# Performance work log

Measured on AMD Instinct MI355X. Metric: run time of the kernel, lower is better.

The kernel has to match this reference:

```python
import jax, jax.numpy as jnp
import numpy as np

N_POINTS = 16
SPHERE_RADIUS = 2.5
BIG = 1e9

def _layernorm(x, g, b, eps=1e-5):
    mu = jnp.mean(x, axis=-1, keepdims=True)
    var = jnp.var(x, axis=-1, keepdims=True)
    return (x - mu) * jax.lax.rsqrt(var + eps) * g + b

def setup_inputs() -> dict:
    key = jax.random.key(0)
    ks = jax.random.split(key, 12)
    R, I, D, L = 1048576, 8, 64, 2
    orig = jax.random.normal(ks[0], (R, 3), jnp.float32)
    vec = jax.random.normal(ks[1], (R, 3), jnp.float32)
    vec = vec / jnp.linalg.norm(vec, axis=-1, keepdims=True)
    t1 = jax.random.uniform(ks[2], (I, R), jnp.float32) * 2.0
    t2 = t1 + jax.random.uniform(ks[3], (I, R), jnp.float32) * 0.5
    mask = jax.random.randint(ks[4], (I, R), 0, 2) > 0
    W_in = jax.random.normal(ks[5], (N_POINTS * 3, D), jnp.float32) * 0.1
    b_in = jnp.zeros((D,), jnp.float32)
    ln_g = jnp.ones((L, D), jnp.float32)
    ln_b = jnp.zeros((L, D), jnp.float32)
    W_mid = jax.random.normal(ks[6], (L, D, D), jnp.float32) * 0.1
    b_mid = jnp.zeros((L, D), jnp.float32)
    W_cls = jax.random.normal(ks[7], (D, 1), jnp.float32) * 0.1
    b_cls = jnp.zeros((1,), jnp.float32)
    W_dist = jax.random.normal(ks[8], (D, 1), jnp.float32) * 0.1
    b_dist = jnp.zeros((1,), jnp.float32)
    return dict(orig=orig, vec=vec, t1=t1, t2=t2, mask=mask,
                W_in=W_in, b_in=b_in, ln_g=ln_g, ln_b=ln_b,
                W_mid=W_mid, b_mid=b_mid, W_cls=W_cls, b_cls=b_cls,
                W_dist=W_dist, b_dist=b_dist)

def reference(orig, vec, t1, t2, mask, W_in, b_in, ln_g, ln_b, W_mid, b_mid,
              W_cls, b_cls, W_dist, b_dist):
    R = orig.shape[0]
    L = W_mid.shape[0]
    ts = jnp.linspace(0.0, 1.0, N_POINTS)  # [P]

    def net(x):  # x: [R, P*3]
        h = x @ W_in + b_in
        for l in range(L):
            h = jax.nn.relu(h)
            h = _layernorm(h, ln_g[l], ln_b[l])
            h = h @ W_mid[l] + b_mid[l]
        h = jax.nn.relu(h)
        cls = (h @ W_cls + b_cls)[:, 0]
        dval = (h @ W_dist + b_dist)[:, 0]
        return cls, dval

    def step(dist, it):
        m_i, t1_i, t2_i = it  # [R]
        dt = t2_i - t1_i
        inp_orig = orig + vec * t1_i[:, None]          # [R,3]
        inp_vec = vec * dt[:, None]                    # [R,3]
        # sample points along segment: [R, P, 3]
        inp = (inp_orig[:, None, :] + inp_vec[:, None, :] * ts[None, :, None]) / SPHERE_RADIUS
        cls, dval = net(inp.reshape(R, -1))
        dval = dval * dt + t1_i
        upd = (cls > 0) & (dval < dist) & m_i
        return jnp.where(upd, dval, dist), None

    dist0 = jnp.full((R,), BIG, jnp.float32)
    dist, _ = jax.lax.scan(step, dist0, (mask, t1, t2))
    dist = jnp.where(dist == BIG, 0.0, dist)
    return (dist > 0, dist)
```

## Files before the change

kernel.cpp:

```cpp
#include <hip/hip_runtime.h>
#include <math.h>

constexpr int   P      = 16;
constexpr int   DIN    = 48;
constexpr int   DH     = 64;
constexpr int   NITER  = 8;
constexpr int   NLAYER = 2;
constexpr float BIGV   = 1e9f;
constexpr float INV_R  = 1.0f / 2.5f;
constexpr int   RLOG   = 20;

typedef float f32x4 __attribute__((ext_vector_type(4)));
typedef const __attribute__((address_space(1))) f32x4 gf4_t;

__device__ __forceinline__ gf4_t* vmem(const float* p) {
    unsigned long long a = (unsigned long long)p;
    asm volatile("" : "+v"(a));
    return (gf4_t*)a;
}

__device__ __forceinline__ unsigned fkey(float f) {
    unsigned b = __float_as_uint(f);
    return (b & 0x80000000u) ? ~b : (b | 0x80000000u);
}
__device__ __forceinline__ float funkey(unsigned k) {
    unsigned b = (k & 0x80000000u) ? (k ^ 0x80000000u) : ~k;
    return __uint_as_float(b);
}

__device__ __noinline__
void slow_eval(const float* __restrict__ orig, const float* __restrict__ vec,
               const float* __restrict__ t1,   const float* __restrict__ t2,
               size_t tidx, unsigned r,
               const float* __restrict__ W_in,  const float* __restrict__ b_in,
               const float* __restrict__ ln_g,  const float* __restrict__ ln_b,
               const float* __restrict__ W_mid, const float* __restrict__ b_mid,
               const float* __restrict__ W_cls, const float* __restrict__ b_cls,
               const float* __restrict__ W_dist,const float* __restrict__ b_dist,
               float& cls_o, float& dval_o)
{
    const float o0 = orig[3*r+0], o1 = orig[3*r+1], o2 = orig[3*r+2];
    const float v0 = vec[3*r+0],  v1 = vec[3*r+1],  v2 = vec[3*r+2];
    const float t1i = t1[tidx], t2i = t2[tidx];

    const float dt  = __fsub_rn(t2i, t1i);
    const float io0 = __fadd_rn(o0, __fmul_rn(v0, t1i));
    const float io1 = __fadd_rn(o1, __fmul_rn(v1, t1i));
    const float io2 = __fadd_rn(o2, __fmul_rn(v2, t1i));
    const float iv0 = __fmul_rn(v0, dt);
    const float iv1 = __fmul_rn(v1, dt);
    const float iv2 = __fmul_rn(v2, dt);
    const float delta = 1.0f / 15.0f;

    float x[DIN];
    #pragma unroll
    for (int p = 0; p < P; ++p) {
        const float tp = __fmul_rn((float)p, delta);
        x[3*p+0] = __fdiv_rn(__fadd_rn(io0, __fmul_rn(iv0, tp)), 2.5f);
        x[3*p+1] = __fdiv_rn(__fadd_rn(io1, __fmul_rn(iv1, tp)), 2.5f);
        x[3*p+2] = __fdiv_rn(__fadd_rn(io2, __fmul_rn(iv2, tp)), 2.5f);
    }

    float a[DH];
    #pragma unroll 1
    for (int d = 0; d < DH; ++d) {
        double acc0 = 0.0, acc1 = 0.0;
        #pragma unroll
        for (int k = 0; k < DIN; k += 2) {
            acc0 = fma((double)x[k],   (double)W_in[k*DH + d],     acc0);
            acc1 = fma((double)x[k+1], (double)W_in[(k+1)*DH + d], acc1);
        }
        a[d] = __fadd_rn((float)(acc0 + acc1), b_in[d]);
    }

    #pragma unroll 1
    for (int l = 0; l < NLAYER; ++l) {
        #pragma unroll 1
        for (int d = 0; d < DH; ++d) a[d] = fmaxf(a[d], 0.0f);

        double s = 0.0;
        #pragma unroll 1
        for (int d = 0; d < DH; ++d) s += (double)a[d];
        const float mu = (float)(s * (1.0 / 64.0));

        double vs = 0.0;
        #pragma unroll 1
        for (int d = 0; d < DH; ++d) {
            const float c = __fsub_rn(a[d], mu);
            vs = fma((double)c, (double)c, vs);
        }
        const float var = (float)(vs * (1.0 / 64.0));
        const float ve  = __fadd_rn(var, 1e-5f);
        const float inv = (float)(1.0 / sqrt((double)ve));

        float hn[DH];
        #pragma unroll 1
        for (int d = 0; d < DH; ++d) {
            float t = __fsub_rn(a[d], mu);
            t = __fmul_rn(t, inv);
            t = __fmul_rn(t, ln_g[l*DH + d]);
            hn[d] = __fadd_rn(t, ln_b[l*DH + d]);
        }

        #pragma unroll 1
        for (int d = 0; d < DH; ++d) {
            double acc0 = 0.0, acc1 = 0.0;
            #pragma unroll
            for (int k = 0; k < DH; k += 2) {
                acc0 = fma((double)hn[k],   (double)W_mid[(l*DH + k)*DH + d],   acc0);
                acc1 = fma((double)hn[k+1], (double)W_mid[(l*DH + k+1)*DH + d], acc1);
            }
            a[d] = __fadd_rn((float)(acc0 + acc1), b_mid[l*DH + d]);
        }
    }

    double c0 = 0.0, c1 = 0.0, d0 = 0.0, d1 = 0.0;
    #pragma unroll 1
    for (int d = 0; d < DH; d += 2) {
        const float h0 = fmaxf(a[d],   0.0f);
        const float h1 = fmaxf(a[d+1], 0.0f);
        c0 = fma((double)h0, (double)W_cls[d],    c0);
        c1 = fma((double)h1, (double)W_cls[d+1],  c1);
        d0 = fma((double)h0, (double)W_dist[d],   d0);
        d1 = fma((double)h1, (double)W_dist[d+1], d1);
    }
    const float cls = __fadd_rn((float)(c0 + c1), b_cls[0]);
    const float dv  = __fadd_rn((float)(d0 + d1), b_dist[0]);
    cls_o  = cls;
    dval_o = __fadd_rn(__fmul_rn(dv, dt), t1i);
}

__global__ __launch_bounds__(256)
void compact_k(const int* __restrict__ mask, unsigned* __restrict__ cnt,
               unsigned* __restrict__ work)
{
    __shared__ unsigned wcnt[4];
    __shared__ unsigned woff[4];

    const int tid  = threadIdx.x;
    const int lane = tid & 63;
    const int wv   = tid >> 6;
    const int idx  = blockIdx.x * 256 + tid;

    const bool m = (mask[idx] != 0);
    const unsigned long long b = __ballot(m);
    const int nact = __popcll(b);
    if (lane == 0) wcnt[wv] = (unsigned)nact;
    __syncthreads();
    if (tid == 0) {
        const unsigned tot = wcnt[0] + wcnt[1] + wcnt[2] + wcnt[3];
        unsigned base = tot ? atomicAdd(cnt, tot) : 0u;
        #pragma unroll
        for (int w = 0; w < 4; ++w) { woff[w] = base; base += wcnt[w]; }
    }
    __syncthreads();
    if (m) {
        const int pre = __popcll(b & ((1ull << lane) - 1ull));
        work[woff[wv] + pre] = (unsigned)idx;
    }
}

__global__ __launch_bounds__(256)
void init_k(unsigned* __restrict__ arena, int R)
{
    const unsigned key_big = fkey(BIGV);
    for (int r = blockIdx.x * 256 + threadIdx.x; r < R; r += gridDim.x * 256)
        arena[r] = key_big;
}

__global__ __launch_bounds__(256)
void finalize_k(float* __restrict__ out, int R)
{
    unsigned* arena = (unsigned*)out + R;
    for (int r = blockIdx.x * 256 + threadIdx.x; r < R; r += gridDim.x * 256) {
        const float dist = funkey(arena[r]);
        const float dfin = (dist == BIGV) ? 0.0f : dist;
        out[r] = (dfin > 0.0f) ? 1.0f : 0.0f;
        ((float*)arena)[r] = dfin;
    }
}

template<bool GLOBAL>
__device__ __forceinline__
void mm_khalf1(const float* Wbase, int kofs, const float* col, float (&a)[DH])
{
    #pragma unroll 2
    for (int k = 0; k < 32; ++k) {
        const float hk = col[k*64];
        if constexpr (GLOBAL) {
            gf4_t* wr = vmem(Wbase + (kofs + k)*DH);
            #pragma unroll
            for (int j = 0; j < 16; ++j) {
                const f32x4 w4 = wr[j];
                a[4*j+0] = fmaf(hk, w4.x, a[4*j+0]);
                a[4*j+1] = fmaf(hk, w4.y, a[4*j+1]);
                a[4*j+2] = fmaf(hk, w4.z, a[4*j+2]);
                a[4*j+3] = fmaf(hk, w4.w, a[4*j+3]);
            }
        } else {
            const f32x4* wr = (const f32x4*)(Wbase + (kofs + k)*DH);
            #pragma unroll
            for (int j = 0; j < 16; ++j) {
                const f32x4 w4 = wr[j];
                a[4*j+0] = fmaf(hk, w4.x, a[4*j+0]);
                a[4*j+1] = fmaf(hk, w4.y, a[4*j+1]);
                a[4*j+2] = fmaf(hk, w4.z, a[4*j+2]);
                a[4*j+3] = fmaf(hk, w4.w, a[4*j+3]);
            }
        }
    }
}

__global__ __launch_bounds__(256, 3)
void main1_k(const float* __restrict__ orig,
             const float* __restrict__ vec,
             const float* __restrict__ t1,
             const float* __restrict__ t2,
             const float* __restrict__ W_in,
             const float* __restrict__ b_in,
             const float* __restrict__ ln_g,
             const float* __restrict__ ln_b,
             const float* __restrict__ W_mid,
             const float* __restrict__ b_mid,
             const float* __restrict__ W_cls,
             const float* __restrict__ b_cls,
             const float* __restrict__ W_dist,
             const float* __restrict__ b_dist,
             const unsigned* __restrict__ work,
             const unsigned* __restrict__ cnt,
             unsigned* __restrict__ arena)
{
    __shared__ __align__(16) float wl0[DH*DH];
    __shared__ __align__(16) float act[4][32][64];

    const int tid  = threadIdx.x;
    const int lane = tid & 63;
    const int wv   = tid >> 6;

    {
        f32x4*       dst = (f32x4*)wl0;
        const f32x4* s2  = (const f32x4*)W_mid;
        #pragma unroll 1
        for (int idx = tid; idx < DH*DH/4; idx += 256) dst[idx] = s2[idx];
    }
    __syncthreads();

    float* col = &act[wv][0][lane];

    const unsigned T    = *cnt;
    const unsigned gtid = blockIdx.x * 256 + tid;
    const unsigned NTOT = gridDim.x * 256;

    for (unsigned g = gtid; g < T; g += NTOT) {
        const unsigned pk = work[g];
        const unsigned r  = pk & 0xFFFFFu;
        const float tt1 = t1[pk], tt2 = t2[pk];
        const float dt  = tt2 - tt1;
        const float o0 = orig[3*r+0], o1 = orig[3*r+1], o2 = orig[3*r+2];
        const float v0 = vec[3*r+0],  v1 = vec[3*r+1],  v2 = vec[3*r+2];
        const float io0 = fmaf(v0, tt1, o0);
        const float io1 = fmaf(v1, tt1, o1);
        const float io2 = fmaf(v2, tt1, o2);
        const float iv0 = v0 * dt, iv1 = v1 * dt, iv2 = v2 * dt;

        float a[DH];
        #pragma unroll
        for (int d = 0; d < DH; ++d) a[d] = 0.0f;

        #pragma unroll 1
        for (int p = 0; p < P; ++p) {
            const float tp = (float)p * (1.0f / 15.0f);
            const float x0 = fmaf(iv0, tp, io0) * INV_R;
            const float x1 = fmaf(iv1, tp, io1) * INV_R;
            const float x2 = fmaf(iv2, tp, io2) * INV_R;
            gf4_t* w0 = vmem(W_in + (3*p+0)*DH);
            gf4_t* w1 = vmem(W_in + (3*p+1)*DH);
            gf4_t* w2 = vmem(W_in + (3*p+2)*DH);
            #pragma unroll
            for (int j = 0; j < 16; ++j) {
                const f32x4 u = w0[j], v4 = w1[j], w4 = w2[j];
                a[4*j+0] = fmaf(x2, w4.x, fmaf(x1, v4.x, fmaf(x0, u.x, a[4*j+0])));
                a[4*j+1] = fmaf(x2, w4.y, fmaf(x1, v4.y, fmaf(x0, u.y, a[4*j+1])));
                a[4*j+2] = fmaf(x2, w4.z, fmaf(x1, v4.z, fmaf(x0, u.z, a[4*j+2])));
                a[4*j+3] = fmaf(x2, w4.w, fmaf(x1, v4.w, fmaf(x0, u.w, a[4*j+3])));
            }
        }
        #pragma unroll
        for (int d = 0; d < DH; ++d) a[d] += b_in[d];

        float invprod = 1.0f;

        #pragma unroll
        for (int l = 0; l < NLAYER; ++l) {
            #pragma unroll
            for (int d = 0; d < DH; ++d) a[d] = fmaxf(a[d], 0.0f);

            float mu = 0.0f;
            #pragma unroll
            for (int d = 0; d < DH; ++d) mu += a[d];
            mu *= (1.0f / 64.0f);

            float var = 0.0f;
            #pragma unroll
            for (int d = 0; d < DH; ++d) {
                const float c = a[d] - mu;
                var = fmaf(c, c, var);
            }
            var *= (1.0f / 64.0f);
            const float inv = 1.0f / sqrtf(var + 1e-5f);
            invprod *= inv;

            const float* gg = ln_g + l*DH;
            const float* bb = ln_b + l*DH;

            #pragma unroll
            for (int d = 0; d < 32; ++d)
                col[d*64] = fmaf((a[d] - mu) * inv, gg[d], bb[d]);
            float hh[32];
            #pragma unroll
            for (int j = 0; j < 32; ++j)
                hh[j] = fmaf((a[32+j] - mu) * inv, gg[32+j], bb[32+j]);

            #pragma unroll
            for (int d = 0; d < DH; ++d) a[d] = 0.0f;

            if (l == 0) mm_khalf1<false>(wl0,            0, col, a);
            else        mm_khalf1<true >(W_mid + DH*DH,  0, col, a);

            #pragma unroll
            for (int j = 0; j < 32; ++j)
                col[j*64] = hh[j];

            if (l == 0) mm_khalf1<false>(wl0,           32, col, a);
            else        mm_khalf1<true >(W_mid + DH*DH, 32, col, a);

            const float* bm = b_mid + l*DH;
            #pragma unroll
            for (int d = 0; d < DH; ++d) a[d] += bm[d];
        }

        #pragma unroll
        for (int d = 0; d < DH; ++d) a[d] = fmaxf(a[d], 0.0f);

        float c0 = 0.f, c1 = 0.f, c2 = 0.f, c3 = 0.f;
        float e0 = 0.f, e1 = 0.f, e2 = 0.f, e3 = 0.f;
        #pragma unroll
        for (int j = 0; j < 16; ++j) {
            c0 = fmaf(a[4*j+0], W_cls[4*j+0],  c0);
            c1 = fmaf(a[4*j+1], W_cls[4*j+1],  c1);
            c2 = fmaf(a[4*j+2], W_cls[4*j+2],  c2);
            c3 = fmaf(a[4*j+3], W_cls[4*j+3],  c3);
            e0 = fmaf(a[4*j+0], W_dist[4*j+0], e0);
            e1 = fmaf(a[4*j+1], W_dist[4*j+1], e1);
            e2 = fmaf(a[4*j+2], W_dist[4*j+2], e2);
            e3 = fmaf(a[4*j+3], W_dist[4*j+3], e3);
        }
        float cls = ((c0 + c1) + (c2 + c3)) + b_cls[0];
        float dv  = ((e0 + e1) + (e2 + e3)) + b_dist[0];
        float dval = fmaf(dv, dt, tt1);

        float thr = 2e-6f * invprod;
        thr = fminf(fmaxf(thr, 3e-5f), 2e-2f);
        if ((fabsf(cls) < thr) || (fabsf(dval) < thr)) {
            slow_eval(orig, vec, t1, t2, (size_t)pk, r,
                      W_in, b_in, ln_g, ln_b, W_mid, b_mid,
                      W_cls, b_cls, W_dist, b_dist, cls, dval);
        }
        if (cls > 0.0f)
            atomicMin(arena + r, fkey(dval));
    }
}

__global__ __launch_bounds__(256, 2)
void fallback_k(const float* __restrict__ orig, const float* __restrict__ vec,
                const float* __restrict__ t1,   const float* __restrict__ t2,
                const int*   __restrict__ mask,
                const float* __restrict__ W_in,  const float* __restrict__ b_in,
                const float* __restrict__ ln_g,  const float* __restrict__ ln_b,
                const float* __restrict__ W_mid, const float* __restrict__ b_mid,
                const float* __restrict__ W_cls, const float* __restrict__ b_cls,
                const float* __restrict__ W_dist,const float* __restrict__ b_dist,
                float* __restrict__ out, int R)
{
    __shared__ __align__(16) float wlds[DIN*DH + NLAYER*DH*DH];
    __shared__ __align__(16) float act[4][32][64];

    const int tid  = threadIdx.x;
    const int lane = tid & 63;
    const int wv   = tid >> 6;

    {
        f32x4*       dst = (f32x4*)wlds;
        const f32x4* s1  = (const f32x4*)W_in;
        const f32x4* s2  = (const f32x4*)W_mid;
        #pragma unroll 1
        for (int idx = tid; idx < DIN*DH/4; idx += 256)        dst[idx] = s1[idx];
        #pragma unroll 1
        for (int idx = tid; idx < NLAYER*DH*DH/4; idx += 256)  dst[DIN*DH/4 + idx] = s2[idx];
    }
    __syncthreads();

    const float* win_l  = wlds;
    const float* wmid_l = wlds + DIN*DH;

    const int r = blockIdx.x * 256 + tid;
    if (r >= R) return;

    float* myact = &act[wv][0][lane];

    const float o0 = orig[3*r+0], o1 = orig[3*r+1], o2 = orig[3*r+2];
    const float v0 = vec[3*r+0],  v1 = vec[3*r+1],  v2 = vec[3*r+2];

    float dist = BIGV;

    #pragma unroll 1
    for (int i = 0; i < NITER; ++i) {
        const float t1i = t1[(size_t)i * R + r];
        const float t2i = t2[(size_t)i * R + r];
        const int   mi  = mask[(size_t)i * R + r];
        if (!mi) continue;
        const float dt = t2i - t1i;

        const float io0 = fmaf(v0, t1i, o0);
        const float io1 = fmaf(v1, t1i, o1);
        const float io2 = fmaf(v2, t1i, o2);
        const float iv0 = v0 * dt, iv1 = v1 * dt, iv2 = v2 * dt;

        float a[DH];
        #pragma unroll
        for (int d = 0; d < DH; ++d) a[d] = 0.0f;

        #pragma unroll 1
        for (int p = 0; p < P; ++p) {
            const float tp = (float)p * (1.0f / 15.0f);
            const float x0 = fmaf(iv0, tp, io0) * INV_R;
            const float x1 = fmaf(iv1, tp, io1) * INV_R;
            const float x2 = fmaf(iv2, tp, io2) * INV_R;
            const f32x4* w0 = (const f32x4*)(win_l + (3*p+0)*DH);
            const f32x4* w1 = (const f32x4*)(win_l + (3*p+1)*DH);
            const f32x4* w2 = (const f32x4*)(win_l + (3*p+2)*DH);
            #pragma unroll
            for (int j = 0; j < 16; ++j) {
                const f32x4 u = w0[j], v4 = w1[j], w4 = w2[j];
                a[4*j+0] = fmaf(x2, w4.x, fmaf(x1, v4.x, fmaf(x0, u.x, a[4*j+0])));
                a[4*j+1] = fmaf(x2, w4.y, fmaf(x1, v4.y, fmaf(x0, u.y, a[4*j+1])));
                a[4*j+2] = fmaf(x2, w4.z, fmaf(x1, v4.z, fmaf(x0, u.z, a[4*j+2])));
                a[4*j+3] = fmaf(x2, w4.w, fmaf(x1, v4.w, fmaf(x0, u.w, a[4*j+3])));
            }
        }
        #pragma unroll
        for (int d = 0; d < DH; ++d) a[d] += b_in[d];

        float invprod = 1.0f;

        #pragma unroll 1
        for (int l = 0; l < NLAYER; ++l) {
            #pragma unroll
            for (int d = 0; d < DH; ++d) a[d] = fmaxf(a[d], 0.0f);

            float mu = 0.0f;
            #pragma unroll
            for (int d = 0; d < DH; ++d) mu += a[d];
            mu *= (1.0f / 64.0f);

            float var = 0.0f;
            #pragma unroll
            for (int d = 0; d < DH; ++d) {
                const float cdev = a[d] - mu;
                var = fmaf(cdev, cdev, var);
            }
            var *= (1.0f / 64.0f);
            const float inv = 1.0f / sqrtf(var + 1e-5f);
            invprod *= inv;

            const float* gp = ln_g + l*DH;
            const float* bp = ln_b + l*DH;

            #pragma unroll
            for (int d = 0; d < 32; ++d)
                myact[d*64] = fmaf((a[d] - mu) * inv, gp[d], bp[d]);
            float hh[32];
            #pragma unroll
            for (int j = 0; j < 32; ++j)
                hh[j] = fmaf((a[32+j] - mu) * inv, gp[32+j], bp[32+j]);

            #pragma unroll
            for (int d = 0; d < DH; ++d) a[d] = 0.0f;

            const float* Wl = wmid_l + l*DH*DH;
            #pragma unroll 4
            for (int k = 0; k < 32; ++k) {
                const float hk = myact[k*64];
                const f32x4* wr = (const f32x4*)(Wl + k*DH);
                #pragma unroll
                for (int j = 0; j < 16; ++j) {
                    const f32x4 w4 = wr[j];
                    a[4*j+0] = fmaf(hk, w4.x, a[4*j+0]);
                    a[4*j+1] = fmaf(hk, w4.y, a[4*j+1]);
                    a[4*j+2] = fmaf(hk, w4.z, a[4*j+2]);
                    a[4*j+3] = fmaf(hk, w4.w, a[4*j+3]);
                }
            }
            #pragma unroll
            for (int j = 0; j < 32; ++j)
                myact[j*64] = hh[j];
            #pragma unroll 4
            for (int k = 32; k < DH; ++k) {
                const float hk = myact[(k-32)*64];
                const f32x4* wr = (const f32x4*)(Wl + k*DH);
                #pragma unroll
                for (int j = 0; j < 16; ++j) {
                    const f32x4 w4 = wr[j];
                    a[4*j+0] = fmaf(hk, w4.x, a[4*j+0]);
                    a[4*j+1] = fmaf(hk, w4.y, a[4*j+1]);
                    a[4*j+2] = fmaf(hk, w4.z, a[4*j+2]);
                    a[4*j+3] = fmaf(hk, w4.w, a[4*j+3]);
                }
            }
            const float* bm = b_mid + l*DH;
            #pragma unroll
            for (int d = 0; d < DH; ++d) a[d] += bm[d];
        }

        #pragma unroll
        for (int d = 0; d < DH; ++d) a[d] = fmaxf(a[d], 0.0f);

        float c0 = 0.f, c1 = 0.f, c2 = 0.f, c3 = 0.f;
        float e0 = 0.f, e1 = 0.f, e2 = 0.f, e3 = 0.f;
        #pragma unroll
        for (int j = 0; j < 16; ++j) {
            c0 = fmaf(a[4*j+0], W_cls[4*j+0],  c0);
            c1 = fmaf(a[4*j+1], W_cls[4*j+1],  c1);
            c2 = fmaf(a[4*j+2], W_cls[4*j+2],  c2);
            c3 = fmaf(a[4*j+3], W_cls[4*j+3],  c3);
            e0 = fmaf(a[4*j+0], W_dist[4*j+0], e0);
            e1 = fmaf(a[4*j+1], W_dist[4*j+1], e1);
            e2 = fmaf(a[4*j+2], W_dist[4*j+2], e2);
            e3 = fmaf(a[4*j+3], W_dist[4*j+3], e3);
        }
        float cls = ((c0 + c1) + (c2 + c3)) + b_cls[0];
        float dv  = ((e0 + e1) + (e2 + e3)) + b_dist[0];
        float dval = fmaf(dv, dt, t1i);

        float thr = 2e-6f * invprod;
        thr = fminf(fmaxf(thr, 3e-5f), 2e-2f);
        if ((fabsf(cls) < thr) || (fabsf(dval) < thr)) {
            slow_eval(orig, vec, t1, t2, (size_t)i * R + r, (unsigned)r,
                      W_in, b_in, ln_g, ln_b, W_mid, b_mid,
                      W_cls, b_cls, W_dist, b_dist, cls, dval);
        }

        if (cls > 0.0f && dval < dist) dist = dval;
    }

    const float dfin = (dist == BIGV) ? 0.0f : dist;
    out[r]     = (dfin > 0.0f) ? 1.0f : 0.0f;
    out[R + r] = dfin;
}

extern "C" void kernel_launch(void* const* d_in, const int* in_sizes, int n_in,
                              void* d_out, int out_size, void* d_ws, size_t ws_size,
                              hipStream_t stream) {
    const float* orig   = (const float*)d_in[0];
    const float* vec    = (const float*)d_in[1];
    const float* t1     = (const float*)d_in[2];
    const float* t2     = (const float*)d_in[3];
    const int*   mask   = (const int*)  d_in[4];
    const float* W_in   = (const float*)d_in[5];
    const float* b_in   = (const float*)d_in[6];
    const float* ln_g   = (const float*)d_in[7];
    const float* ln_b   = (const float*)d_in[8];
    const float* W_mid  = (const float*)d_in[9];
    const float* b_mid  = (const float*)d_in[10];
    const float* W_cls  = (const float*)d_in[11];
    const float* b_cls  = (const float*)d_in[12];
    const float* W_dist = (const float*)d_in[13];
    const float* b_dist = (const float*)d_in[14];

    float* out = (float*)d_out;
    const int R = in_sizes[0] / 3;

    const size_t need_ws = 16 + 4ull * (size_t)R * NITER;
    const bool fast = (R == (1 << RLOG)) && (ws_size >= need_ws);

    if (fast) {
        unsigned* cnt   = (unsigned*)d_ws;
        unsigned* work  = (unsigned*)d_ws + 4;
        unsigned* arena = (unsigned*)d_out + R;

        hipMemsetAsync(cnt, 0, 4, stream);
        compact_k<<<(R * NITER) / 256, 256, 0, stream>>>(mask, cnt, work);
        init_k<<<1024, 256, 0, stream>>>(arena, R);
        main1_k<<<4096, 256, 0, stream>>>(orig, vec, t1, t2,
                                          W_in, b_in, ln_g, ln_b, W_mid, b_mid,
                                          W_cls, b_cls, W_dist, b_dist,
                                          work, cnt, arena);
        finalize_k<<<1024, 256, 0, stream>>>(out, R);
    } else {
        const int threads = 256;
        const int blocks  = (R + threads - 1) / threads;
        fallback_k<<<blocks, threads, 0, stream>>>(
            orig, vec, t1, t2, mask,
            W_in, b_in, ln_g, ln_b, W_mid, b_mid,
            W_cls, b_cls, W_dist, b_dist,
            out, R);
    }
}
```

Measured before the change: 5.250 ms.

## Collapse input layer into precomputed per-axis weight sums

Because sample points are affine in t, the 48-wide input matmul reduces to six 64-wide precomputed vectors (sum of W_in rows and t-weighted sums) built by a small prep kernel. This cuts about 3072 FMAs per ray down to about 384. The change also drops the shared-memory copy of W_mid in favour of direct global loads with a full 64-row activation buffer, lowers the occupancy hint and grid size, and raises the slow-path precision threshold. The reassociated sum changes rounding, so the higher threshold sends more near-boundary rays to the exact slow evaluation.

```diff
diff --git a/kernel.cpp b/kernel.cpp
--- a/kernel.cpp
+++ b/kernel.cpp
@@ -11,13 +11,8 @@
 constexpr int   RLOG   = 20;
 
 typedef float f32x4 __attribute__((ext_vector_type(4)));
-typedef const __attribute__((address_space(1))) f32x4 gf4_t;
-
-__device__ __forceinline__ gf4_t* vmem(const float* p) {
-    unsigned long long a = (unsigned long long)p;
-    asm volatile("" : "+v"(a));
-    return (gf4_t*)a;
-}
+
+__device__ __align__(16) float g_uv[6 * DH];
 
 __device__ __forceinline__ unsigned fkey(float f) {
     unsigned b = __float_as_uint(f);
@@ -180,38 +175,26 @@
     }
 }
 
-template<bool GLOBAL>
-__device__ __forceinline__
-void mm_khalf1(const float* Wbase, int kofs, const float* col, float (&a)[DH])
-{
-    #pragma unroll 2
-    for (int k = 0; k < 32; ++k) {
-        const float hk = col[k*64];
-        if constexpr (GLOBAL) {
-            gf4_t* wr = vmem(Wbase + (kofs + k)*DH);
-            #pragma unroll
-            for (int j = 0; j < 16; ++j) {
-                const f32x4 w4 = wr[j];
-                a[4*j+0] = fmaf(hk, w4.x, a[4*j+0]);
-                a[4*j+1] = fmaf(hk, w4.y, a[4*j+1]);
-                a[4*j+2] = fmaf(hk, w4.z, a[4*j+2]);
-                a[4*j+3] = fmaf(hk, w4.w, a[4*j+3]);
-            }
-        } else {
-            const f32x4* wr = (const f32x4*)(Wbase + (kofs + k)*DH);
-            #pragma unroll
-            for (int j = 0; j < 16; ++j) {
-                const f32x4 w4 = wr[j];
-                a[4*j+0] = fmaf(hk, w4.x, a[4*j+0]);
-                a[4*j+1] = fmaf(hk, w4.y, a[4*j+1]);
-                a[4*j+2] = fmaf(hk, w4.z, a[4*j+2]);
-                a[4*j+3] = fmaf(hk, w4.w, a[4*j+3]);
-            }
-        }
-    }
-}
-
-__global__ __launch_bounds__(256, 3)
+__global__ __launch_bounds__(256)
+void prepuv_k(const float* __restrict__ W_in)
+{
+    const int id = blockIdx.x * 256 + threadIdx.x;
+    if (id >= 6 * DH) return;
+    const int c  = id / DH;
+    const int d  = id % DH;
+    const int cc = (c >= 3) ? c - 3 : c;
+    const bool isV = (c >= 3);
+    float s = 0.0f;
+    #pragma unroll
+    for (int p = 0; p < P; ++p) {
+        const float tp = (float)p * (1.0f / 15.0f);
+        const float w  = W_in[(3*p + cc)*DH + d];
+        s = isV ? fmaf(tp, w, s) : (s + w);
+    }
+    g_uv[id] = s;
+}
+
+__global__ __launch_bounds__(256, 2)
 void main1_k(const float* __restrict__ orig,
              const float* __restrict__ vec,
              const float* __restrict__ t1,
@@ -230,20 +213,11 @@
              const unsigned* __restrict__ cnt,
              unsigned* __restrict__ arena)
 {
-    __shared__ __align__(16) float wl0[DH*DH];
-    __shared__ __align__(16) float act[4][32][64];
+    __shared__ float act[4][DH][64];
 
     const int tid  = threadIdx.x;
     const int lane = tid & 63;
     const int wv   = tid >> 6;
-
-    {
-        f32x4*       dst = (f32x4*)wl0;
-        const f32x4* s2  = (const f32x4*)W_mid;
-        #pragma unroll 1
-        for (int idx = tid; idx < DH*DH/4; idx += 256) dst[idx] = s2[idx];
-    }
-    __syncthreads();
 
     float* col = &act[wv][0][lane];
 
@@ -264,29 +238,32 @@
         const float iv0 = v0 * dt, iv1 = v1 * dt, iv2 = v2 * dt;
 
         float a[DH];
-        #pragma unroll
-        for (int d = 0; d < DH; ++d) a[d] = 0.0f;
-
-        #pragma unroll 1
-        for (int p = 0; p < P; ++p) {
-            const float tp = (float)p * (1.0f / 15.0f);
-            const float x0 = fmaf(iv0, tp, io0) * INV_R;
-            const float x1 = fmaf(iv1, tp, io1) * INV_R;
-            const float x2 = fmaf(iv2, tp, io2) * INV_R;
-            gf4_t* w0 = vmem(W_in + (3*p+0)*DH);
-            gf4_t* w1 = vmem(W_in + (3*p+1)*DH);
-            gf4_t* w2 = vmem(W_in + (3*p+2)*DH);
+
+        {
+            const f32x4* U0 = (const f32x4*)(g_uv + 0*DH);
+            const f32x4* U1 = (const f32x4*)(g_uv + 1*DH);
+            const f32x4* U2 = (const f32x4*)(g_uv + 2*DH);
+            const f32x4* V0 = (const f32x4*)(g_uv + 3*DH);
+            const f32x4* V1 = (const f32x4*)(g_uv + 4*DH);
+            const f32x4* V2 = (const f32x4*)(g_uv + 5*DH);
+            const f32x4* B  = (const f32x4*)b_in;
             #pragma unroll
             for (int j = 0; j < 16; ++j) {
-                const f32x4 u = w0[j], v4 = w1[j], w4 = w2[j];
-                a[4*j+0] = fmaf(x2, w4.x, fmaf(x1, v4.x, fmaf(x0, u.x, a[4*j+0])));
-                a[4*j+1] = fmaf(x2, w4.y, fmaf(x1, v4.y, fmaf(x0, u.y, a[4*j+1])));
-                a[4*j+2] = fmaf(x2, w4.z, fmaf(x1, v4.z, fmaf(x0, u.z, a[4*j+2])));
-                a[4*j+3] = fmaf(x2, w4.w, fmaf(x1, v4.w, fmaf(x0, u.w, a[4*j+3])));
-            }
-        }
-        #pragma unroll
-        for (int d = 0; d < DH; ++d) a[d] += b_in[d];
+                const f32x4 u0 = U0[j], u1 = U1[j], u2 = U2[j];
+                const f32x4 w0 = V0[j], w1 = V1[j], w2 = V2[j];
+                const f32x4 bb = B[j];
+                #pragma unroll
+                for (int q = 0; q < 4; ++q) {
+                    float s = io0 * u0[q];
+                    s = fmaf(io1, u1[q], s);
+                    s = fmaf(io2, u2[q], s);
+                    s = fmaf(iv0, w0[q], s);
+                    s = fmaf(iv1, w1[q], s);
+                    s = fmaf(iv2, w2[q], s);
+                    a[4*j+q] = fmaf(s, INV_R, bb[q]);
+                }
+            }
+        }
 
         float invprod = 1.0f;
 
@@ -314,26 +291,26 @@
             const float* bb = ln_b + l*DH;
 
             #pragma unroll
-            for (int d = 0; d < 32; ++d)
+            for (int d = 0; d < DH; ++d)
                 col[d*64] = fmaf((a[d] - mu) * inv, gg[d], bb[d]);
-            float hh[32];
-            #pragma unroll
-            for (int j = 0; j < 32; ++j)
-                hh[j] = fmaf((a[32+j] - mu) * inv, gg[32+j], bb[32+j]);
 
             #pragma unroll
             for (int d = 0; d < DH; ++d) a[d] = 0.0f;
 
-            if (l == 0) mm_khalf1<false>(wl0,            0, col, a);
-            else        mm_khalf1<true >(W_mid + DH*DH,  0, col, a);
-
-            #pragma unroll
-            for (int j = 0; j < 32; ++j)
-                col[j*64] = hh[j];
-
-            if (l == 0) mm_khalf1<false>(wl0,           32, col, a);
-            else        mm_khalf1<true >(W_mid + DH*DH, 32, col, a);
-
+            const float* Wl = W_mid + l*DH*DH;
+            #pragma unroll 2
+            for (int k = 0; k < DH; ++k) {
+                const float hk = col[k*64];
+                const f32x4* wr = (const f32x4*)(Wl + k*DH);
+                #pragma unroll
+                for (int j = 0; j < 16; ++j) {
+                    const f32x4 w4 = wr[j];
+                    a[4*j+0] = fmaf(hk, w4.x, a[4*j+0]);
+                    a[4*j+1] = fmaf(hk, w4.y, a[4*j+1]);
+                    a[4*j+2] = fmaf(hk, w4.z, a[4*j+2]);
+                    a[4*j+3] = fmaf(hk, w4.w, a[4*j+3]);
+                }
+            }
             const float* bm = b_mid + l*DH;
             #pragma unroll
             for (int d = 0; d < DH; ++d) a[d] += bm[d];
@@ -360,7 +337,7 @@
         float dval = fmaf(dv, dt, tt1);
 
         float thr = 2e-6f * invprod;
-        thr = fminf(fmaxf(thr, 3e-5f), 2e-2f);
+        thr = fminf(fmaxf(thr, 3e-4f), 2e-2f);
         if ((fabsf(cls) < thr) || (fabsf(dval) < thr)) {
             slow_eval(orig, vec, t1, t2, (size_t)pk, r,
                       W_in, b_in, ln_g, ln_b, W_mid, b_mid,
@@ -590,8 +567,9 @@
 
         hipMemsetAsync(cnt, 0, 4, stream);
         compact_k<<<(R * NITER) / 256, 256, 0, stream>>>(mask, cnt, work);
+        prepuv_k<<<2, 256, 0, stream>>>(W_in);
         init_k<<<1024, 256, 0, stream>>>(arena, R);
-        main1_k<<<4096, 256, 0, stream>>>(orig, vec, t1, t2,
+        main1_k<<<2048, 256, 0, stream>>>(orig, vec, t1, t2,
                                           W_in, b_in, ln_g, ln_b, W_mid, b_mid,
                                           W_cls, b_cls, W_dist, b_dist,
                                           work, cnt, arena);
```

New measurement: 6.786 ms. +29.3%, slower.

## Collapse input layer into 6x64 precomputed linear map over origin and direction

Applied to the files above, without the earlier changes.

Because the sampled points are linear in t, the 48-wide input matmul reduces to six precomputed 64-vectors, sum_p W and sum_p t_p W per coordinate. A tiny prep kernel builds these each call, so the first layer costs 6 FMAs per output instead of 48. The rounding now differs from the reference order, so the threshold for the exact slow re-evaluation is raised to send more borderline cases to it.

```diff
diff --git a/kernel.cpp b/kernel.cpp
--- a/kernel.cpp
+++ b/kernel.cpp
@@ -12,6 +12,8 @@
 
 typedef float f32x4 __attribute__((ext_vector_type(4)));
 typedef const __attribute__((address_space(1))) f32x4 gf4_t;
+
+__device__ __align__(16) float g_uv[6 * DH];
 
 __device__ __forceinline__ gf4_t* vmem(const float* p) {
     unsigned long long a = (unsigned long long)p;
@@ -178,6 +180,25 @@
         out[r] = (dfin > 0.0f) ? 1.0f : 0.0f;
         ((float*)arena)[r] = dfin;
     }
+}
+
+__global__ __launch_bounds__(256)
+void prepuv_k(const float* __restrict__ W_in)
+{
+    const int id = blockIdx.x * 256 + threadIdx.x;
+    if (id >= 6 * DH) return;
+    const int c  = id / DH;
+    const int d  = id % DH;
+    const int cc = (c >= 3) ? c - 3 : c;
+    const bool isV = (c >= 3);
+    float s = 0.0f;
+    #pragma unroll
+    for (int p = 0; p < P; ++p) {
+        const float tp = (float)p * (1.0f / 15.0f);
+        const float w  = W_in[(3*p + cc)*DH + d];
+        s = isV ? fmaf(tp, w, s) : (s + w);
+    }
+    g_uv[id] = s;
 }
 
 template<bool GLOBAL>
@@ -264,29 +285,32 @@
         const float iv0 = v0 * dt, iv1 = v1 * dt, iv2 = v2 * dt;
 
         float a[DH];
-        #pragma unroll
-        for (int d = 0; d < DH; ++d) a[d] = 0.0f;
-
-        #pragma unroll 1
-        for (int p = 0; p < P; ++p) {
-            const float tp = (float)p * (1.0f / 15.0f);
-            const float x0 = fmaf(iv0, tp, io0) * INV_R;
-            const float x1 = fmaf(iv1, tp, io1) * INV_R;
-            const float x2 = fmaf(iv2, tp, io2) * INV_R;
-            gf4_t* w0 = vmem(W_in + (3*p+0)*DH);
-            gf4_t* w1 = vmem(W_in + (3*p+1)*DH);
-            gf4_t* w2 = vmem(W_in + (3*p+2)*DH);
+
+        {
+            const f32x4* U0 = (const f32x4*)(g_uv + 0*DH);
+            const f32x4* U1 = (const f32x4*)(g_uv + 1*DH);
+            const f32x4* U2 = (const f32x4*)(g_uv + 2*DH);
+            const f32x4* V0 = (const f32x4*)(g_uv + 3*DH);
+            const f32x4* V1 = (const f32x4*)(g_uv + 4*DH);
+            const f32x4* V2 = (const f32x4*)(g_uv + 5*DH);
+            const f32x4* B  = (const f32x4*)b_in;
             #pragma unroll
             for (int j = 0; j < 16; ++j) {
-                const f32x4 u = w0[j], v4 = w1[j], w4 = w2[j];
-                a[4*j+0] = fmaf(x2, w4.x, fmaf(x1, v4.x, fmaf(x0, u.x, a[4*j+0])));
-                a[4*j+1] = fmaf(x2, w4.y, fmaf(x1, v4.y, fmaf(x0, u.y, a[4*j+1])));
-                a[4*j+2] = fmaf(x2, w4.z, fmaf(x1, v4.z, fmaf(x0, u.z, a[4*j+2])));
-                a[4*j+3] = fmaf(x2, w4.w, fmaf(x1, v4.w, fmaf(x0, u.w, a[4*j+3])));
-            }
-        }
-        #pragma unroll
-        for (int d = 0; d < DH; ++d) a[d] += b_in[d];
+                const f32x4 u0 = U0[j], u1 = U1[j], u2 = U2[j];
+                const f32x4 w0 = V0[j], w1 = V1[j], w2 = V2[j];
+                const f32x4 bb = B[j];
+                #pragma unroll
+                for (int q = 0; q < 4; ++q) {
+                    float s = io0 * u0[q];
+                    s = fmaf(io1, u1[q], s);
+                    s = fmaf(io2, u2[q], s);
+                    s = fmaf(iv0, w0[q], s);
+                    s = fmaf(iv1, w1[q], s);
+                    s = fmaf(iv2, w2[q], s);
+                    a[4*j+q] = fmaf(s, INV_R, bb[q]);
+                }
+            }
+        }
 
         float invprod = 1.0f;
 
@@ -360,7 +384,7 @@
         float dval = fmaf(dv, dt, tt1);
 
         float thr = 2e-6f * invprod;
-        thr = fminf(fmaxf(thr, 3e-5f), 2e-2f);
+        thr = fminf(fmaxf(thr, 3e-4f), 2e-2f);
         if ((fabsf(cls) < thr) || (fabsf(dval) < thr)) {
             slow_eval(orig, vec, t1, t2, (size_t)pk, r,
                       W_in, b_in, ln_g, ln_b, W_mid, b_mid,
@@ -590,6 +614,7 @@
 
         hipMemsetAsync(cnt, 0, 4, stream);
         compact_k<<<(R * NITER) / 256, 256, 0, stream>>>(mask, cnt, work);
+        prepuv_k<<<2, 256, 0, stream>>>(W_in);
         init_k<<<1024, 256, 0, stream>>>(arena, R);
         main1_k<<<4096, 256, 0, stream>>>(orig, vec, t1, t2,
                                           W_in, b_in, ln_g, ln_b, W_mid, b_mid,
```

Result: slower. 9.463 ms (+80.3%).
